# Optimization experiments

Hardware: AMD Instinct MI355X
Metric: run time of the kernel (lower is better)

Reference implementation:

```python
import jax, jax.numpy as jnp
import numpy as np

B, N, M = 4, 1024, 3072          # batch, latent (query) len, prefix context len
D, H, DH, L, F = 512, 8, 64, 6, 2048  # dim, heads, dim_head, depth, ff hidden
SCALE = DH ** -0.5


def _ln(x, g, b):
    m = jnp.mean(x, axis=-1, keepdims=True)
    v = jnp.mean(jnp.square(x - m), axis=-1, keepdims=True)
    return (x - m) * jax.lax.rsqrt(v + 1e-5) * g + b


def _heads(t):  # [b, n, h*d] -> [b, h, n, d]
    b, n, _ = t.shape
    return t.reshape(b, n, H, DH).transpose(0, 2, 1, 3)


def _attend(q, k, v):
    # q:[b,h,i,d], k/v:[b,h,j,d]; causal mask triu(j-i+1) as in source
    i, j = q.shape[2], k.shape[2]
    sim = jnp.einsum('bhid,bhjd->bhij', q * SCALE, k)
    mask = jnp.triu(jnp.ones((i, j), dtype=bool), j - i + 1)
    sim = jnp.where(mask, -jnp.finfo(sim.dtype).max, sim)
    attn = jax.nn.softmax(sim, axis=-1)
    out = jnp.einsum('bhij,bhjd->bhid', attn, v)
    return out.transpose(0, 2, 1, 3).reshape(q.shape[0], i, H * DH)


def _ff(x, g, b, w1, w2):
    return jax.nn.gelu(_ln(x, g, b) @ w1, approximate=False) @ w2


def setup_inputs() -> dict:
    key = jax.random.key(0)
    ks = jax.random.split(key, 12)
    rn = lambda k, shape: jax.random.normal(k, shape, dtype=jnp.float32) * 0.02
    return {
        'x': jax.random.normal(ks[0], (B, N, D), jnp.float32),
        'context': jax.random.normal(ks[1], (B, M, D), jnp.float32),
        'pa_norm_g': jnp.ones((D,), jnp.float32), 'pa_norm_b': jnp.zeros((D,), jnp.float32),
        'pa_cnorm_g': jnp.ones((D,), jnp.float32), 'pa_cnorm_b': jnp.zeros((D,), jnp.float32),
        'pa_wq': rn(ks[2], (D, H * DH)), 'pa_wkv': rn(ks[3], (D, 2 * H * DH)),
        'pa_wo': rn(ks[4], (H * DH, D)), 'pa_wo_b': jnp.zeros((D,), jnp.float32),
        'pf_ln_g': jnp.ones((D,), jnp.float32), 'pf_ln_b': jnp.zeros((D,), jnp.float32),
        'pf_w1': rn(ks[5], (D, F)), 'pf_w2': rn(ks[6], (F, D)),
        'sa_ln_g': jnp.ones((L, D), jnp.float32), 'sa_ln_b': jnp.zeros((L, D), jnp.float32),
        'sa_wqkv': rn(ks[7], (L, D, 3 * H * DH)), 'sa_wo': rn(ks[8], (L, H * DH, D)),
        'sf_ln_g': jnp.ones((L, D), jnp.float32), 'sf_ln_b': jnp.zeros((L, D), jnp.float32),
        'sf_w1': rn(ks[9], (L, D, F)), 'sf_w2': rn(ks[10], (L, F, D)),
    }


def reference(x, context, pa_norm_g, pa_norm_b, pa_cnorm_g, pa_cnorm_b,
              pa_wq, pa_wkv, pa_wo, pa_wo_b, pf_ln_g, pf_ln_b, pf_w1, pf_w2,
              sa_ln_g, sa_ln_b, sa_wqkv, sa_wo, sf_ln_g, sf_ln_b, sf_w1, sf_w2):
    # --- CausalPrefixAttention (eval mode: no dropout, context_mask=None) ---
    xn = _ln(x, pa_norm_g, pa_norm_b)
    cn = _ln(context, pa_cnorm_g, pa_cnorm_b)
    q = _heads(xn @ pa_wq)
    k_in, v_in = jnp.split(xn @ pa_wkv, 2, axis=-1)
    k_c, v_c = jnp.split(cn @ pa_wkv, 2, axis=-1)
    k = _heads(jnp.concatenate([k_c, k_in], axis=1))  # [b,h,M+N,d]
    v = _heads(jnp.concatenate([v_c, v_in], axis=1))
    x = _attend(q, k, v) @ pa_wo + pa_wo_b + x
    x = _ff(x, pf_ln_g, pf_ln_b, pf_w1, pf_w2) + x
    # --- depth x (CausalAttention + FeedForward) ---
    for l in range(L):
        xn = _ln(x, sa_ln_g[l], sa_ln_b[l])
        qq, kk, vv = jnp.split(xn @ sa_wqkv[l], 3, axis=-1)
        x = _attend(_heads(qq), _heads(kk), _heads(vv)) @ sa_wo[l] + x
        x = _ff(x, sf_ln_g[l], sf_ln_b[l], sf_w1[l], sf_w2[l]) + x
    return x
```

## Files before the change

### kernel.cpp

```cpp
#include <hip/hip_runtime.h>
#include <hip/hip_bf16.h>
#include <cstdint>
#include <cstddef>

typedef __bf16 bf16;
typedef __attribute__((ext_vector_type(8))) __bf16 bf16x8;
typedef __attribute__((ext_vector_type(4))) __bf16 bf16x4;
typedef __attribute__((ext_vector_type(4))) float f32x4;

constexpr int B_ = 4, QN = 1024, MCTX = 3072, D_ = 512, H_ = 8, DHE = 64, L_ = 6, FF_ = 2048;
constexpr float SCL2_ = 0.18033688011f;

__device__ __forceinline__ f32x4 mfma16(bf16x8 a, bf16x8 b, f32x4 c) {
  return __builtin_amdgcn_mfma_f32_16x16x32_bf16(a, b, c, 0, 0, 0);
}

__device__ __forceinline__ void gl_lds16(const bf16* g, bf16* l) {
  __builtin_amdgcn_global_load_lds((const __attribute__((address_space(1))) void*)g,
                                   (__attribute__((address_space(3))) void*)l, 16, 0, 0);
}

__device__ __forceinline__ float fexp2(float x) {
  float r;
  asm("v_exp_f32 %0, %1" : "=v"(r) : "v"(x));
  return r;
}

__global__ __launch_bounds__(256) void ln_kernel(const float* __restrict__ x,
                                                 const float* __restrict__ g,
                                                 const float* __restrict__ b,
                                                 bf16* __restrict__ out, int rows) {
  int wid = threadIdx.x >> 6, lane = threadIdx.x & 63;
  int row = blockIdx.x * 4 + wid;
  if (row >= rows) return;
  const float* xr = x + (size_t)row * D_;
  f32x4 a0 = *(const f32x4*)(xr + lane * 8);
  f32x4 a1 = *(const f32x4*)(xr + lane * 8 + 4);
  float s = 0.f;
#pragma unroll
  for (int i = 0; i < 4; i++) { s += a0[i]; s += a1[i]; }
#pragma unroll
  for (int d = 1; d < 64; d <<= 1) s += __shfl_xor(s, d);
  float mean = s * (1.0f / 512.0f);
  float q = 0.f;
#pragma unroll
  for (int i = 0; i < 4; i++) {
    float t0 = a0[i] - mean, t1 = a1[i] - mean;
    q += t0 * t0 + t1 * t1;
  }
#pragma unroll
  for (int d = 1; d < 64; d <<= 1) q += __shfl_xor(q, d);
  float rstd = rsqrtf(q * (1.0f / 512.0f) + 1e-5f);
  f32x4 g0 = *(const f32x4*)(g + lane * 8);
  f32x4 g1 = *(const f32x4*)(g + lane * 8 + 4);
  f32x4 b0 = *(const f32x4*)(b + lane * 8);
  f32x4 b1 = *(const f32x4*)(b + lane * 8 + 4);
  bf16x8 o;
#pragma unroll
  for (int i = 0; i < 4; i++) {
    o[i] = (bf16)((a0[i] - mean) * rstd * g0[i] + b0[i]);
    o[i + 4] = (bf16)((a1[i] - mean) * rstd * g1[i] + b1[i]);
  }
  *(bf16x8*)(out + (size_t)row * D_ + lane * 8) = o;
}

struct WDesc { const float* src; bf16* dst; int K; int N; int tstart; };
struct WPack { WDesc d[30]; int n; };

__global__ __launch_bounds__(256) void wtrans_all(WPack p) {
  __shared__ float tile[64][65];
  const int bid = blockIdx.x;
  int mi = 0;
  for (int i = 1; i < p.n; i++)
    if (p.d[i].tstart <= bid) mi = i;
  const float* src = p.d[mi].src;
  bf16* dst = p.d[mi].dst;
  const int K = p.d[mi].K, N = p.d[mi].N;
  const int lt = bid - p.d[mi].tstart;
  const int ntx = N >> 6;
  const int n0 = (lt % ntx) * 64, k0 = (lt / ntx) * 64;
  const int tx = threadIdx.x, ty = threadIdx.y;
#pragma unroll
  for (int pp = 0; pp < 16; pp++)
    tile[pp * 4 + ty][tx] = src[(size_t)(k0 + pp * 4 + ty) * N + n0 + tx];
  __syncthreads();
#pragma unroll
  for (int pp = 0; pp < 16; pp++)
    dst[(size_t)(n0 + pp * 4 + ty) * K + k0 + tx] = (bf16)tile[tx][pp * 4 + ty];
}

template <int EPI>
__global__ __launch_bounds__(256) void gemm128(const bf16* __restrict__ A,
                                               const bf16* __restrict__ BT,
                                               void* __restrict__ C0,
                                               void* __restrict__ C1,
                                               void* __restrict__ C2,
                                               const float* __restrict__ resid,
                                               const float* __restrict__ bias,
                                               int M, int N, int K, int vstr) {
  __shared__ bf16 smA[2][128 * 64];
  __shared__ bf16 smB[2][128 * 64];
  const int tid = threadIdx.x, wid = tid >> 6, lane = tid & 63;
  const int lr = lane & 15, lg = lane >> 4;
  const int tm = blockIdx.y * 128, tn = blockIdx.x * 128;
  const int wr = (wid >> 1) * 64, wc = (wid & 1) * 64;

  const int l3 = lane >> 3;
  const int kslot = ((lane & 7) ^ l3) * 8;
  const bf16* gA[4];
  const bf16* gB[4];
#pragma unroll
  for (int j = 0; j < 4; j++) {
    gA[j] = A + (size_t)(tm + wid * 32 + j * 8 + l3) * K + kslot;
    gB[j] = BT + (size_t)(tn + wid * 32 + j * 8 + l3) * K + kslot;
  }

  f32x4 acc[4][4] = {};
  const int nt = K >> 6;

  auto stage = [&](int bi, int kt) {
#pragma unroll
    for (int j = 0; j < 4; j++) {
      gl_lds16(gA[j] + kt, &smA[bi][(wid * 32 + j * 8) * 64]);
      gl_lds16(gB[j] + kt, &smB[bi][(wid * 32 + j * 8) * 64]);
    }
  };

  stage(0, 0);
  int buf = 0;
  for (int t = 0; t < nt; ++t) {
    asm volatile("s_waitcnt vmcnt(0)" ::: "memory");
    __builtin_amdgcn_s_barrier();
    __builtin_amdgcn_sched_barrier(0);
    if (t + 1 < nt) stage(buf ^ 1, (t + 1) * 64);

    bf16x8 af[4][2], bfr[4][2];
#pragma unroll
    for (int i = 0; i < 4; i++) {
      const int row = wr + i * 16 + lr;
#pragma unroll
      for (int kk = 0; kk < 2; kk++)
        af[i][kk] = *(const bf16x8*)(&smA[buf][row * 64 + (((kk * 4 + lg) ^ (row & 7)) * 8)]);
    }
#pragma unroll
    for (int j = 0; j < 4; j++) {
      const int row = wc + j * 16 + lr;
#pragma unroll
      for (int kk = 0; kk < 2; kk++)
        bfr[j][kk] = *(const bf16x8*)(&smB[buf][row * 64 + (((kk * 4 + lg) ^ (row & 7)) * 8)]);
    }
#pragma unroll
    for (int kk = 0; kk < 2; kk++)
#pragma unroll
      for (int i = 0; i < 4; i++)
#pragma unroll
        for (int j = 0; j < 4; j++)
          acc[i][j] = mfma16(af[i][kk], bfr[j][kk], acc[i][j]);
    buf ^= 1;
  }

  const bool row_major_dst =
      (EPI == 1) || (EPI == 3 && tn < 1024) || (EPI == 4 && tn < 1024) || (EPI == 5 && tn < 512);
  if (row_major_dst) {
    bf16* dst;
    int dstr, rbase, coff;
    if (EPI == 1) { dst = (bf16*)C0; dstr = N; rbase = tm; coff = tn; }
    else if (EPI == 3) {
      if (tn < 512) { dst = (bf16*)C0; dstr = 512; rbase = tm; coff = tn; }
      else { dst = (bf16*)C1; dstr = 1024; rbase = (tm >> 10) * 4096 + (tm & 1023) + 3072; coff = tn - 512; }
    } else if (EPI == 4) { dst = (bf16*)C0; dstr = 1536; rbase = tm; coff = tn; }
    else { dst = (bf16*)C1; dstr = 1024; rbase = (tm / 3072) * 4096 + (tm % 3072); coff = tn; }

    __syncthreads();
    bf16* lb = &smA[0][0];
#pragma unroll
    for (int i = 0; i < 4; i++) {
#pragma unroll
      for (int r = 0; r < 4; r++) {
        const int row = wr + i * 16 + lg * 4 + r;
#pragma unroll
        for (int j = 0; j < 4; j++) {
          const int col = wc + j * 16 + lr;
          float v = acc[i][j][r];
          if (EPI == 1) {
            float u = v * (0.7978845608f + 0.0356774081f * v * v);
            float e = fexp2(fminf(2.885390082f * u, 80.0f));
            v = v * e / (1.0f + e);
          }
          lb[row * 128 + (col ^ ((row & 7) << 3))] = (bf16)v;
        }
      }
    }
    __syncthreads();
#pragma unroll
    for (int p = 0; p < 8; p++) {
      const int row = p * 16 + (tid >> 4);
      const int cb = (tid & 15) * 8;
      bf16x8 v = *(const bf16x8*)&lb[row * 128 + (cb ^ ((row & 7) << 3))];
      *(bf16x8*)&dst[(size_t)(rbase + row) * dstr + coff + cb] = v;
    }
  } else {
#pragma unroll
    for (int i = 0; i < 4; i++) {
      const int row = tm + wr + i * 16 + lg * 4;
#pragma unroll
      for (int j = 0; j < 4; j++) {
        const int col = tn + wc + j * 16 + lr;
        bf16x4 pk = {(bf16)acc[i][j][0], (bf16)acc[i][j][1],
                     (bf16)acc[i][j][2], (bf16)acc[i][j][3]};
        if (EPI == 3) {
          const int cc = col - 1024, hh = cc >> 6, dh = cc & 63;
          const int bb = row >> 10, s = (row & 1023) + 3072;
          *(bf16x4*)&((bf16*)C2)[((size_t)(bb * 8 + hh) * 64 + dh) * vstr + s] = pk;
        } else if (EPI == 4) {
          const int cc = col - 1024, hh = cc >> 6, dh = cc & 63;
          const int bb = row >> 10, s = row & 1023;
          *(bf16x4*)&((bf16*)C2)[((size_t)(bb * 8 + hh) * 64 + dh) * vstr + s] = pk;
        } else {
          const int bq = row / 3072, s = row - bq * 3072;
          const int cc = col - 512, hh = cc >> 6, dh = cc & 63;
          *(bf16x4*)&((bf16*)C2)[((size_t)(bq * 8 + hh) * 64 + dh) * vstr + s] = pk;
        }
      }
    }
  }
}

__global__ __launch_bounds__(256) void gemm64_res(const bf16* __restrict__ A,
                                                  const bf16* __restrict__ BT,
                                                  float* __restrict__ Cout,
                                                  const float* __restrict__ resid,
                                                  const float* __restrict__ bias,
                                                  int M, int N, int K) {
  __shared__ bf16 smA[3][64 * 64];
  __shared__ bf16 smB[3][64 * 64];
  const int tid = threadIdx.x, wid = tid >> 6, lane = tid & 63;
  const int lr = lane & 15, lg = lane >> 4;
  const int tm = blockIdx.y * 64, tn = blockIdx.x * 64;
  const int wr = (wid >> 1) * 32, wc = (wid & 1) * 32;

  const int l3 = lane >> 3;
  const int kslot = ((lane & 7) ^ l3) * 8;
  const int row0 = 2 * wid * 8 + l3;
  const bf16* gA0 = A + (size_t)(tm + row0) * K + kslot;
  const bf16* gA1 = A + (size_t)(tm + row0 + 8) * K + kslot;
  const bf16* gB0 = BT + (size_t)(tn + row0) * K + kslot;
  const bf16* gB1 = BT + (size_t)(tn + row0 + 8) * K + kslot;

  f32x4 acc[2][2] = {};
  const int nt = K >> 6;

  auto stage = [&](int bi, int kt) {
    gl_lds16(gA0 + kt, &smA[bi][(2 * wid) * 512]);
    gl_lds16(gA1 + kt, &smA[bi][(2 * wid + 1) * 512]);
    gl_lds16(gB0 + kt, &smB[bi][(2 * wid) * 512]);
    gl_lds16(gB1 + kt, &smB[bi][(2 * wid + 1) * 512]);
  };

  stage(0, 0);
  if (nt > 1) stage(1, 64);

  for (int t = 0; t < nt; ++t) {
    const int bi = t % 3;
    if (t + 1 < nt) {
      asm volatile("s_waitcnt vmcnt(4)" ::: "memory");
    } else {
      asm volatile("s_waitcnt vmcnt(0)" ::: "memory");
    }
    __builtin_amdgcn_s_barrier();
    __builtin_amdgcn_sched_barrier(0);
    if (t + 2 < nt) stage((t + 2) % 3, (t + 2) * 64);

    bf16x8 af[2][2], bfr[2][2];
#pragma unroll
    for (int i = 0; i < 2; i++) {
      const int row = wr + i * 16 + lr;
#pragma unroll
      for (int kk = 0; kk < 2; kk++)
        af[i][kk] = *(const bf16x8*)(&smA[bi][row * 64 + (((kk * 4 + lg) ^ (row & 7)) * 8)]);
    }
#pragma unroll
    for (int j = 0; j < 2; j++) {
      const int row = wc + j * 16 + lr;
#pragma unroll
      for (int kk = 0; kk < 2; kk++)
        bfr[j][kk] = *(const bf16x8*)(&smB[bi][row * 64 + (((kk * 4 + lg) ^ (row & 7)) * 8)]);
    }
#pragma unroll
    for (int kk = 0; kk < 2; kk++)
#pragma unroll
      for (int i = 0; i < 2; i++)
#pragma unroll
        for (int j = 0; j < 2; j++)
          acc[i][j] = mfma16(af[i][kk], bfr[j][kk], acc[i][j]);
  }

  __syncthreads();
  float* lbuf = (float*)&smA[0][0];
#pragma unroll
  for (int i = 0; i < 2; i++) {
#pragma unroll
    for (int r = 0; r < 4; r++) {
      const int row = wr + i * 16 + lg * 4 + r;
#pragma unroll
      for (int j = 0; j < 2; j++)
        lbuf[row * 68 + wc + j * 16 + lr] = acc[i][j][r];
    }
  }
  __syncthreads();
#pragma unroll
  for (int p = 0; p < 4; p++) {
    const int row = p * 16 + (tid >> 4);
    const int col = (tid & 15) * 4;
    f32x4 v = *(const f32x4*)&lbuf[row * 68 + col];
    const size_t gidx = (size_t)(tm + row) * N + tn + col;
    f32x4 rs = *(const f32x4*)&resid[gidx];
    if (bias) {
      f32x4 bs = *(const f32x4*)&bias[tn + col];
#pragma unroll
      for (int e = 0; e < 4; e++) v[e] += bs[e];
    }
#pragma unroll
    for (int e = 0; e < 4; e++) v[e] += rs[e];
    *(f32x4*)&Cout[gidx] = v;
  }
}

template <int NSPLIT>
__global__ __launch_bounds__(256) void attn_kernel(const bf16* __restrict__ q, int qstride,
                                                   const bf16* __restrict__ k, int kstride,
                                                   const bf16* __restrict__ vt,
                                                   bf16* __restrict__ out,
                                                   bf16* __restrict__ po,
                                                   float* __restrict__ pm,
                                                   float* __restrict__ pl,
                                                   int Skv, int Moff, int spllen) {
  __shared__ bf16 kls[2][4096];
  __shared__ bf16 vls[2][4096];
  __shared__ bf16 pls[4][1024];

  const int tid = threadIdx.x, wid = tid >> 6, lane = tid & 63;
  const int lr = lane & 15, lg = lane >> 4, lg4 = lg * 4;
  const int b = blockIdx.z, h = blockIdx.y;
  const int qblk = blockIdx.x / NSPLIT;
  const int split = blockIdx.x % NSPLIT;
  const int q0b = qblk * 64;
  const int q0w = q0b + wid * 16;
  const int kv_lo = split * spllen;

  int jhi_blk = Moff + q0b + 63;
  if (jhi_blk > Skv - 1) jhi_blk = Skv - 1;
  int hi = kv_lo + spllen;
  if (hi > jhi_blk + 1) hi = jhi_blk + 1;
  const int ntl = (hi > kv_lo) ? ((hi - kv_lo + 63) >> 6) : 0;

  if (NSPLIT > 1 && ntl == 0) {
    size_t rb = ((size_t)split * B_ * H_ + (size_t)b * H_ + h) * QN + q0w;
    const int row = lane >> 2;
    bf16x8 z = {};
#pragma unroll
    for (int half = 0; half < 2; half++)
      *(bf16x8*)&po[(rb + row) * 64 + (lane & 3) * 16 + half * 8] = z;
    if (lg == 0) { pm[rb + lr] = -3e38f; pl[rb + lr] = 0.f; }
    return;
  }

  const int ss = (tid >> 6) & 1;
  const int sel = ss * 32 + ((tid >> 4) & 3) * 8;
  const int srow0 = (tid >> 7) * 16 + (tid & 15);
  const bf16* kbase = k + (size_t)b * Skv * kstride + h * DHE + sel;
  const bf16* vbase = vt + (size_t)((b * H_ + h) * DHE) * Skv + sel;

  const bf16* qp = q + (size_t)(b * QN + q0w + lr) * qstride + h * DHE;
  bf16x8 qa0 = *(const bf16x8*)(qp + lg * 8);
  bf16x8 qa1 = *(const bf16x8*)(qp + 32 + lg * 8);
#pragma unroll
  for (int i = 0; i < 8; i++) {
    qa0[i] = (bf16)((float)qa0[i] * SCL2_);
    qa1[i] = (bf16)((float)qa1[i] * SCL2_);
  }

  f32x4 o[4] = {};
  float lrun = 0.f;

  auto stage = [&](int bi, int j0) {
    gl_lds16(kbase + (size_t)(j0 + srow0) * kstride, &kls[bi][wid * 512]);
    gl_lds16(kbase + (size_t)(j0 + srow0 + 32) * kstride, &kls[bi][2048 + wid * 512]);
    gl_lds16(vbase + (size_t)srow0 * Skv + j0, &vls[bi][wid * 512]);
    gl_lds16(vbase + (size_t)(srow0 + 32) * Skv + j0, &vls[bi][2048 + wid * 512]);
  };

  stage(0, kv_lo);
  __syncthreads();
  int buf = 0;
  bf16* pw = &pls[wid][0];

  for (int t = 0; t < ntl; ++t) {
    const int j0 = kv_lo + t * 64;
    if (t + 1 < ntl) stage(buf ^ 1, j0 + 64);
    const bf16* kbp = &kls[buf][0];
    const bf16* vbp = &vls[buf][0];

    f32x4 sv[4];
    __builtin_amdgcn_s_setprio(1);
#pragma unroll
    for (int kg = 0; kg < 4; kg++) {
      bf16x8 k0 = *(const bf16x8*)(kbp + (kg * 128 + lane) * 8);
      bf16x8 k1 = *(const bf16x8*)(kbp + (kg * 128 + 64 + lane) * 8);
      f32x4 z = {0.f, 0.f, 0.f, 0.f};
      z = mfma16(k0, qa0, z);
      z = mfma16(k1, qa1, z);
      sv[kg] = z;
    }
    __builtin_amdgcn_s_setprio(0);
    const bool full = (j0 + 63 <= Moff + q0w);
    if (!full) {
      const int limq = Moff + q0w + lr;
#pragma unroll
      for (int kg = 0; kg < 4; kg++)
#pragma unroll
        for (int r = 0; r < 4; r++)
          if (j0 + kg * 16 + lg4 + r > limq) sv[kg][r] = -3e38f;
    }
    float rsum = 0.f;
#pragma unroll
    for (int kg = 0; kg < 4; kg++) {
      float p0 = fexp2(sv[kg][0]);
      float p1 = fexp2(sv[kg][1]);
      float p2 = fexp2(sv[kg][2]);
      float p3 = fexp2(sv[kg][3]);
      rsum += (p0 + p1) + (p2 + p3);
      bf16x4 pk = {(bf16)p0, (bf16)p1, (bf16)p2, (bf16)p3};
      const int k8 = kg * 2 + (lg >> 1);
      *(bf16x4*)(pw + ((k8 >> 2) * 64 + (k8 & 3) * 16 + lr) * 8 + (lg & 1) * 4) = pk;
    }
    rsum += __shfl_xor(rsum, 16);
    rsum += __shfl_xor(rsum, 32);
    lrun += rsum;
    bf16x8 pa0 = *(const bf16x8*)(pw + lane * 8);
    bf16x8 pa1 = *(const bf16x8*)(pw + (64 + lane) * 8);
    __builtin_amdgcn_s_setprio(1);
#pragma unroll
    for (int f = 0; f < 4; f++) {
      bf16x8 v0 = *(const bf16x8*)(vbp + (f * 128 + lane) * 8);
      bf16x8 v1 = *(const bf16x8*)(vbp + (f * 128 + 64 + lane) * 8);
      o[f] = mfma16(pa0, v0, o[f]);
      o[f] = mfma16(pa1, v1, o[f]);
    }
    __builtin_amdgcn_s_setprio(0);
    __syncthreads();
    buf ^= 1;
  }

  if (NSPLIT == 1) {
    float linv = 1.0f / lrun;
    float li[4];
#pragma unroll
    for (int r = 0; r < 4; r++) li[r] = __shfl(linv, lg4 + r);
#pragma unroll
    for (int f = 0; f < 4; f++)
#pragma unroll
      for (int r = 0; r < 4; r++) {
        const int row = lg4 + r, col = f * 16 + lr;
        pw[row * 64 + (col ^ ((row & 7) << 3))] = (bf16)(o[f][r] * li[r]);
      }
    const int row = lane >> 2;
#pragma unroll
    for (int half = 0; half < 2; half++) {
      const int cb = (lane & 3) * 16 + half * 8;
      bf16x8 v = *(const bf16x8*)&pw[row * 64 + (cb ^ ((row & 7) << 3))];
      *(bf16x8*)&out[(size_t)(b * QN + q0w + row) * D_ + h * DHE + cb] = v;
    }
  } else {
    size_t rb = ((size_t)split * B_ * H_ + (size_t)b * H_ + h) * QN + q0w;
#pragma unroll
    for (int f = 0; f < 4; f++)
#pragma unroll
      for (int r = 0; r < 4; r++) {
        const int row = lg4 + r, col = f * 16 + lr;
        pw[row * 64 + (col ^ ((row & 7) << 3))] = (bf16)o[f][r];
      }
    const int row = lane >> 2;
#pragma unroll
    for (int half = 0; half < 2; half++) {
      const int cb = (lane & 3) * 16 + half * 8;
      bf16x8 v = *(const bf16x8*)&pw[row * 64 + (cb ^ ((row & 7) << 3))];
      *(bf16x8*)&po[(rb + row) * 64 + cb] = v;
    }
    if (lg == 0) { pm[rb + lr] = 0.f; pl[rb + lr] = lrun; }
  }
}

template <int NSPLIT>
__global__ __launch_bounds__(256) void attn_combine(const bf16* __restrict__ po,
                                                    const float* __restrict__ pm,
                                                    const float* __restrict__ pl,
                                                    bf16* __restrict__ out) {
  constexpr int TOT = B_ * H_ * QN;
  const int wid = threadIdx.x >> 6, lane = threadIdx.x & 63;
  const int row = blockIdx.x * 4 + wid;
  float mv[NSPLIT], lv[NSPLIT];
  float mstar = -3e38f;
#pragma unroll
  for (int s = 0; s < NSPLIT; s++) {
    mv[s] = pm[s * TOT + row];
    lv[s] = pl[s * TOT + row];
    mstar = fmaxf(mstar, mv[s]);
  }
  float lstar = 0.f, acc = 0.f;
#pragma unroll
  for (int s = 0; s < NSPLIT; s++) {
    float w = fexp2(mv[s] - mstar);
    lstar += lv[s] * w;
    acc += (float)po[((size_t)s * TOT + row) * 64 + lane] * w;
  }
  const int b = row >> 13, hq = row & 8191, h = hq >> 10, qq = hq & 1023;
  out[((size_t)b * QN + qq) * D_ + h * DHE + lane] = (bf16)(acc / lstar);
}

extern "C" void kernel_launch(void* const* d_in, const int* in_sizes, int n_in,
                              void* d_out, int out_size, void* d_ws, size_t ws_size,
                              hipStream_t stream) {
  const float* x       = (const float*)d_in[0];
  const float* ctx     = (const float*)d_in[1];
  const float* pa_ng   = (const float*)d_in[2];
  const float* pa_nb   = (const float*)d_in[3];
  const float* pa_cg   = (const float*)d_in[4];
  const float* pa_cb   = (const float*)d_in[5];
  const float* pa_wq   = (const float*)d_in[6];
  const float* pa_wkv  = (const float*)d_in[7];
  const float* pa_wo   = (const float*)d_in[8];
  const float* pa_wob  = (const float*)d_in[9];
  const float* pf_g    = (const float*)d_in[10];
  const float* pf_b    = (const float*)d_in[11];
  const float* pf_w1   = (const float*)d_in[12];
  const float* pf_w2   = (const float*)d_in[13];
  const float* sa_g    = (const float*)d_in[14];
  const float* sa_b    = (const float*)d_in[15];
  const float* sa_wqkv = (const float*)d_in[16];
  const float* sa_wo   = (const float*)d_in[17];
  const float* sf_g    = (const float*)d_in[18];
  const float* sf_b    = (const float*)d_in[19];
  const float* sf_w1   = (const float*)d_in[20];
  const float* sf_w2   = (const float*)d_in[21];
  float* xo = (float*)d_out;

  char* ws = (char*)d_ws;
  size_t off = 0;
  auto alloc = [&](size_t bytes) -> char* {
    char* p = ws + off;
    off += (bytes + 255) & ~(size_t)255;
    return p;
  };

  bf16* wqT    = (bf16*)alloc((size_t)512 * 512 * 2);
  bf16* wkvT   = (bf16*)alloc((size_t)1024 * 512 * 2);
  bf16* woT    = (bf16*)alloc((size_t)512 * 512 * 2);
  bf16* w1T    = (bf16*)alloc((size_t)2048 * 512 * 2);
  bf16* w2T    = (bf16*)alloc((size_t)512 * 2048 * 2);
  bf16* saqkvT = (bf16*)alloc((size_t)L_ * 1536 * 512 * 2);
  bf16* sawoT  = (bf16*)alloc((size_t)L_ * 512 * 512 * 2);
  bf16* sfw1T  = (bf16*)alloc((size_t)L_ * 2048 * 512 * 2);
  bf16* sfw2T  = (bf16*)alloc((size_t)L_ * 512 * 2048 * 2);
  bf16* xn    = (bf16*)alloc((size_t)4096 * 512 * 2);
  bf16* reg1  = (bf16*)alloc((size_t)12288 * 512 * 2);
  bf16* qb    = (bf16*)alloc((size_t)4096 * 512 * 2);
  bf16* reg2  = (bf16*)alloc((size_t)B_ * 4096 * 1024 * 2);
  bf16* vtb   = (bf16*)alloc((size_t)B_ * H_ * 64 * 4096 * 2);
  bf16* attnb = (bf16*)alloc((size_t)4096 * 512 * 2);
  constexpr int NSPL = 4;
  constexpr int TOTR = B_ * H_ * QN;
  bf16* po = (bf16*)alloc((size_t)NSPL * TOTR * 64 * 2);
  float* pmb = (float*)alloc((size_t)NSPL * TOTR * 4);
  float* plb = (float*)alloc((size_t)NSPL * TOTR * 4);
  const bool use_split = (off <= ws_size);
  bf16* cn = reg1;
  bf16* qkvb = reg1;
  bf16* kvb = reg2;
  bf16* ffh = reg2;
  (void)in_sizes; (void)n_in; (void)out_size;

  WPack wp;
  int nt_acc = 0, wi = 0;
  auto addw = [&](const float* s, bf16* d, int K, int N) {
    wp.d[wi].src = s; wp.d[wi].dst = d; wp.d[wi].K = K; wp.d[wi].N = N;
    wp.d[wi].tstart = nt_acc;
    nt_acc += (N / 64) * (K / 64);
    wi++;
  };
  addw(pa_wq, wqT, 512, 512);
  addw(pa_wkv, wkvT, 512, 1024);
  addw(pa_wo, woT, 512, 512);
  addw(pf_w1, w1T, 512, 2048);
  addw(pf_w2, w2T, 2048, 512);
  for (int l = 0; l < L_; l++) {
    addw(sa_wqkv + (size_t)l * 512 * 1536, saqkvT + (size_t)l * 1536 * 512, 512, 1536);
    addw(sa_wo + (size_t)l * 512 * 512, sawoT + (size_t)l * 512 * 512, 512, 512);
    addw(sf_w1 + (size_t)l * 512 * 2048, sfw1T + (size_t)l * 2048 * 512, 512, 2048);
    addw(sf_w2 + (size_t)l * 2048 * 512, sfw2T + (size_t)l * 512 * 2048, 2048, 512);
  }
  wp.n = wi;
  wtrans_all<<<nt_acc, dim3(64, 4, 1), 0, stream>>>(wp);

  ln_kernel<<<1024, 256, 0, stream>>>(x, pa_ng, pa_nb, xn, 4096);
  ln_kernel<<<3072, 256, 0, stream>>>(ctx, pa_cg, pa_cb, cn, 12288);
  hipLaunchKernelGGL(HIP_KERNEL_NAME(gemm128<5>), dim3(1024 / 128, 12288 / 128), dim3(256), 0,
                     stream, cn, wkvT, nullptr, kvb, vtb, nullptr, nullptr, 12288, 1024, 512, 4096);
  hipLaunchKernelGGL(HIP_KERNEL_NAME(gemm128<3>), dim3(1536 / 128, 4096 / 128), dim3(256), 0,
                     stream, xn, wqT, qb, kvb, vtb, nullptr, nullptr, 4096, 1536, 512, 4096);
  if (use_split) {
    hipLaunchKernelGGL(HIP_KERNEL_NAME(attn_kernel<NSPL>), dim3((QN / 64) * NSPL, H_, B_), dim3(256), 0,
                       stream, qb, 512, kvb, 1024, vtb, attnb, po, pmb, plb, 4096, MCTX, 1024);
    hipLaunchKernelGGL(HIP_KERNEL_NAME(attn_combine<NSPL>), dim3(TOTR / 4), dim3(256), 0,
                       stream, po, pmb, plb, attnb);
  } else {
    hipLaunchKernelGGL(HIP_KERNEL_NAME(attn_kernel<1>), dim3(QN / 64, H_, B_), dim3(256), 0,
                       stream, qb, 512, kvb, 1024, vtb, attnb, po, pmb, plb, 4096, MCTX, 4096);
  }
  gemm64_res<<<dim3(512 / 64, 4096 / 64), 256, 0, stream>>>(attnb, woT, xo, x, pa_wob, 4096, 512, 512);
  ln_kernel<<<1024, 256, 0, stream>>>(xo, pf_g, pf_b, xn, 4096);
  hipLaunchKernelGGL(HIP_KERNEL_NAME(gemm128<1>), dim3(2048 / 128, 4096 / 128), dim3(256), 0,
                     stream, xn, w1T, ffh, nullptr, nullptr, nullptr, nullptr, 4096, 2048, 512, 0);
  gemm64_res<<<dim3(512 / 64, 4096 / 64), 256, 0, stream>>>(ffh, w2T, xo, xo, nullptr, 4096, 512, 2048);

  for (int l = 0; l < L_; l++) {
    ln_kernel<<<1024, 256, 0, stream>>>(xo, sa_g + l * 512, sa_b + l * 512, xn, 4096);
    hipLaunchKernelGGL(HIP_KERNEL_NAME(gemm128<4>), dim3(1536 / 128, 4096 / 128), dim3(256), 0,
                       stream, xn, saqkvT + (size_t)l * 1536 * 512, qkvb, nullptr, vtb,
                       nullptr, nullptr, 4096, 1536, 512, 1024);
    if (use_split) {
      hipLaunchKernelGGL(HIP_KERNEL_NAME(attn_kernel<2>), dim3((QN / 64) * 2, H_, B_), dim3(256), 0,
                         stream, qkvb, 1536, qkvb + 512, 1536, vtb, attnb, po, pmb, plb, 1024, 0, 512);
      hipLaunchKernelGGL(HIP_KERNEL_NAME(attn_combine<2>), dim3(TOTR / 4), dim3(256), 0,
                         stream, po, pmb, plb, attnb);
    } else {
      hipLaunchKernelGGL(HIP_KERNEL_NAME(attn_kernel<1>), dim3(QN / 64, H_, B_), dim3(256), 0,
                         stream, qkvb, 1536, qkvb + 512, 1536, vtb, attnb, po, pmb, plb, 1024, 0, 1024);
    }
    gemm64_res<<<dim3(512 / 64, 4096 / 64), 256, 0, stream>>>(attnb, sawoT + (size_t)l * 512 * 512,
                                                              xo, xo, nullptr, 4096, 512, 512);
    ln_kernel<<<1024, 256, 0, stream>>>(xo, sf_g + l * 512, sf_b + l * 512, xn, 4096);
    hipLaunchKernelGGL(HIP_KERNEL_NAME(gemm128<1>), dim3(2048 / 128, 4096 / 128), dim3(256), 0,
                       stream, xn, sfw1T + (size_t)l * 2048 * 512, ffh, nullptr, nullptr,
                       nullptr, nullptr, 4096, 2048, 512, 0);
    gemm64_res<<<dim3(512 / 64, 4096 / 64), 256, 0, stream>>>(ffh, sfw2T + (size_t)l * 512 * 2048,
                                                              xo, xo, nullptr, 4096, 512, 2048);
  }
}
```

Baseline: 810.5 us.

## Double attention query tile to 128 rows and compute row sums via MFMA

Result: faster. 771.2 us (-4.9%).

```diff
diff --git a/kernel.cpp b/kernel.cpp
--- a/kernel.cpp
+++ b/kernel.cpp
@@ -327,7 +327,7 @@
 }
 
 template <int NSPLIT>
-__global__ __launch_bounds__(256) void attn_kernel(const bf16* __restrict__ q, int qstride,
+__global__ __launch_bounds__(512) void attn_kernel(const bf16* __restrict__ q, int qstride,
                                                    const bf16* __restrict__ k, int kstride,
                                                    const bf16* __restrict__ vt,
                                                    bf16* __restrict__ out,
@@ -337,18 +337,18 @@
                                                    int Skv, int Moff, int spllen) {
   __shared__ bf16 kls[2][4096];
   __shared__ bf16 vls[2][4096];
-  __shared__ bf16 pls[4][1024];
+  __shared__ bf16 pls[8][1024];
 
   const int tid = threadIdx.x, wid = tid >> 6, lane = tid & 63;
   const int lr = lane & 15, lg = lane >> 4, lg4 = lg * 4;
   const int b = blockIdx.z, h = blockIdx.y;
   const int qblk = blockIdx.x / NSPLIT;
   const int split = blockIdx.x % NSPLIT;
-  const int q0b = qblk * 64;
+  const int q0b = qblk * 128;
   const int q0w = q0b + wid * 16;
   const int kv_lo = split * spllen;
 
-  int jhi_blk = Moff + q0b + 63;
+  int jhi_blk = Moff + q0b + 127;
   if (jhi_blk > Skv - 1) jhi_blk = Skv - 1;
   int hi = kv_lo + spllen;
   if (hi > jhi_blk + 1) hi = jhi_blk + 1;
@@ -365,8 +365,7 @@
     return;
   }
 
-  const int ss = (tid >> 6) & 1;
-  const int sel = ss * 32 + ((tid >> 4) & 3) * 8;
+  const int sel = ((tid >> 6) & 1) * 32 + ((tid >> 4) & 3) * 8;
   const int srow0 = (tid >> 7) * 16 + (tid & 15);
   const bf16* kbase = k + (size_t)b * Skv * kstride + h * DHE + sel;
   const bf16* vbase = vt + (size_t)((b * H_ + h) * DHE) * Skv + sel;
@@ -379,15 +378,16 @@
     qa0[i] = (bf16)((float)qa0[i] * SCL2_);
     qa1[i] = (bf16)((float)qa1[i] * SCL2_);
   }
+  bf16x8 vones;
+#pragma unroll
+  for (int i = 0; i < 8; i++) vones[i] = (bf16)1.0f;
 
   f32x4 o[4] = {};
-  float lrun = 0.f;
+  f32x4 o4 = {};
 
   auto stage = [&](int bi, int j0) {
-    gl_lds16(kbase + (size_t)(j0 + srow0) * kstride, &kls[bi][wid * 512]);
-    gl_lds16(kbase + (size_t)(j0 + srow0 + 32) * kstride, &kls[bi][2048 + wid * 512]);
-    gl_lds16(vbase + (size_t)srow0 * Skv + j0, &vls[bi][wid * 512]);
-    gl_lds16(vbase + (size_t)(srow0 + 32) * Skv + j0, &vls[bi][2048 + wid * 512]);
+    gl_lds16(kbase + (size_t)(j0 + srow0) * kstride, &kls[bi][tid * 8]);
+    gl_lds16(vbase + (size_t)srow0 * Skv + j0, &vls[bi][tid * 8]);
   };
 
   stage(0, kv_lo);
@@ -422,21 +422,16 @@
         for (int r = 0; r < 4; r++)
           if (j0 + kg * 16 + lg4 + r > limq) sv[kg][r] = -3e38f;
     }
-    float rsum = 0.f;
 #pragma unroll
     for (int kg = 0; kg < 4; kg++) {
       float p0 = fexp2(sv[kg][0]);
       float p1 = fexp2(sv[kg][1]);
       float p2 = fexp2(sv[kg][2]);
       float p3 = fexp2(sv[kg][3]);
-      rsum += (p0 + p1) + (p2 + p3);
       bf16x4 pk = {(bf16)p0, (bf16)p1, (bf16)p2, (bf16)p3};
       const int k8 = kg * 2 + (lg >> 1);
       *(bf16x4*)(pw + ((k8 >> 2) * 64 + (k8 & 3) * 16 + lr) * 8 + (lg & 1) * 4) = pk;
     }
-    rsum += __shfl_xor(rsum, 16);
-    rsum += __shfl_xor(rsum, 32);
-    lrun += rsum;
     bf16x8 pa0 = *(const bf16x8*)(pw + lane * 8);
     bf16x8 pa1 = *(const bf16x8*)(pw + (64 + lane) * 8);
     __builtin_amdgcn_s_setprio(1);
@@ -447,16 +442,17 @@
       o[f] = mfma16(pa0, v0, o[f]);
       o[f] = mfma16(pa1, v1, o[f]);
     }
+    o4 = mfma16(pa0, vones, o4);
+    o4 = mfma16(pa1, vones, o4);
     __builtin_amdgcn_s_setprio(0);
     __syncthreads();
     buf ^= 1;
   }
 
   if (NSPLIT == 1) {
-    float linv = 1.0f / lrun;
     float li[4];
 #pragma unroll
-    for (int r = 0; r < 4; r++) li[r] = __shfl(linv, lg4 + r);
+    for (int r = 0; r < 4; r++) li[r] = 1.0f / o4[r];
 #pragma unroll
     for (int f = 0; f < 4; f++)
 #pragma unroll
@@ -487,7 +483,13 @@
       bf16x8 v = *(const bf16x8*)&pw[row * 64 + (cb ^ ((row & 7) << 3))];
       *(bf16x8*)&po[(rb + row) * 64 + cb] = v;
     }
-    if (lg == 0) { pm[rb + lr] = 0.f; pl[rb + lr] = lrun; }
+    if (lr == 0) {
+#pragma unroll
+      for (int r = 0; r < 4; r++) {
+        pm[rb + lg4 + r] = 0.f;
+        pl[rb + lg4 + r] = o4[r];
+      }
+    }
   }
 }
 
@@ -609,12 +611,12 @@
   hipLaunchKernelGGL(HIP_KERNEL_NAME(gemm128<3>), dim3(1536 / 128, 4096 / 128), dim3(256), 0,
                      stream, xn, wqT, qb, kvb, vtb, nullptr, nullptr, 4096, 1536, 512, 4096);
   if (use_split) {
-    hipLaunchKernelGGL(HIP_KERNEL_NAME(attn_kernel<NSPL>), dim3((QN / 64) * NSPL, H_, B_), dim3(256), 0,
+    hipLaunchKernelGGL(HIP_KERNEL_NAME(attn_kernel<NSPL>), dim3((QN / 128) * NSPL, H_, B_), dim3(512), 0,
                        stream, qb, 512, kvb, 1024, vtb, attnb, po, pmb, plb, 4096, MCTX, 1024);
     hipLaunchKernelGGL(HIP_KERNEL_NAME(attn_combine<NSPL>), dim3(TOTR / 4), dim3(256), 0,
                        stream, po, pmb, plb, attnb);
   } else {
-    hipLaunchKernelGGL(HIP_KERNEL_NAME(attn_kernel<1>), dim3(QN / 64, H_, B_), dim3(256), 0,
+    hipLaunchKernelGGL(HIP_KERNEL_NAME(attn_kernel<1>), dim3(QN / 128, H_, B_), dim3(512), 0,
                        stream, qb, 512, kvb, 1024, vtb, attnb, po, pmb, plb, 4096, MCTX, 4096);
   }
   gemm64_res<<<dim3(512 / 64, 4096 / 64), 256, 0, stream>>>(attnb, woT, xo, x, pa_wob, 4096, 512, 512);
@@ -629,12 +631,12 @@
                        stream, xn, saqkvT + (size_t)l * 1536 * 512, qkvb, nullptr, vtb,
                        nullptr, nullptr, 4096, 1536, 512, 1024);
     if (use_split) {
-      hipLaunchKernelGGL(HIP_KERNEL_NAME(attn_kernel<2>), dim3((QN / 64) * 2, H_, B_), dim3(256), 0,
+      hipLaunchKernelGGL(HIP_KERNEL_NAME(attn_kernel<2>), dim3((QN / 128) * 2, H_, B_), dim3(512), 0,
                          stream, qkvb, 1536, qkvb + 512, 1536, vtb, attnb, po, pmb, plb, 1024, 0, 512);
       hipLaunchKernelGGL(HIP_KERNEL_NAME(attn_combine<2>), dim3(TOTR / 4), dim3(256), 0,
                          stream, po, pmb, plb, attnb);
     } else {
-      hipLaunchKernelGGL(HIP_KERNEL_NAME(attn_kernel<1>), dim3(QN / 64, H_, B_), dim3(256), 0,
+      hipLaunchKernelGGL(HIP_KERNEL_NAME(attn_kernel<1>), dim3(QN / 128, H_, B_), dim3(512), 0,
                          stream, qkvb, 1536, qkvb + 512, 1536, vtb, attnb, po, pmb, plb, 1024, 0, 1024);
     }
     gemm64_res<<<dim3(512 / 64, 4096 / 64), 256, 0, stream>>>(attnb, sawoT + (size_t)l * 512 * 512,
```
